# Kernel tuning notes

Measured on AMD Instinct MI355X. Metric: run time of the kernel, lower is better.

Reference implementation:

```python
import jax, jax.numpy as jnp
import numpy as np

DIM = 256   # state dimension
T = 8192    # number of time steps
B = 32      # batch of initial conditions
DT = 0.01   # time-grid spacing


def make_A(dim):
    # Faithful to MagnusLadder.__init__: diag=-0.1, superdiag=+0.5, subdiag=-0.5
    A = np.zeros((dim, dim), dtype=np.float32)
    np.fill_diagonal(A, -0.1)
    idx = np.arange(dim - 1)
    A[idx, idx + 1] = 0.5
    A[idx + 1, idx] = -0.5
    return jnp.asarray(A)


def setup_inputs() -> dict:
    key = jax.random.key(0)
    x0 = jax.random.normal(key, (DIM, B), dtype=jnp.float32)
    t = jnp.arange(T, dtype=jnp.float32) * DT  # uniform time grid, dt = DT
    A = make_A(DIM)
    return {"t": t, "x0": x0, "A": A}


def reference(t, x0, A):
    dt = t[1] - t[0]
    expAdt = jax.scipy.linalg.expm(A * dt)  # [dim, dim]

    def step(x, _):
        x = expAdt @ x  # [dim, B]
        return x, x

    _, traj = jax.lax.scan(step, x0, None, length=T - 1)  # [T-1, dim, B]
    return jnp.concatenate([x0[None], traj], axis=0)       # [T, dim, B]
```

## Files before the change

kernel.cpp:

```cpp
#include <hip/hip_runtime.h>
#include <hip/hip_bf16.h>


#define DIMN 256
#define BB   32
#define TSTEPS 8192
#define KT   32
#define DTF  0.01f

typedef __attribute__((ext_vector_type(8))) short bf16x8;
typedef __attribute__((ext_vector_type(4))) float f32x4;

static __device__ __forceinline__ short f2bf(float f) {
    union { __hip_bfloat16 h; short s; } u;
    u.h = __float2bfloat16(f);
    return u.s;
}

__global__ __launch_bounds__(256) void k1_prep(const float* __restrict__ x0,
                                               unsigned short* __restrict__ vfold,
                                               float* __restrict__ yr,
                                               float* __restrict__ yi) {
    const float PI257 = (float)(3.14159265358979323846 / 257.0);
    const float S257  = sqrtf(2.0f / 257.0f);
    const int g = blockIdx.x;
    const int t = threadIdx.x;

    __shared__ float x0s[256 * 32];
    __shared__ float ve[256], vo[256];
    __shared__ float psr[8][32], psi[8][32];

    if (g < 256) {
        const int j = g, J = j >> 1, p = j & 1, m = t;
        const int n = ((j + 1) * (m + 1)) % 514;
        const float v = S257 * sinf((float)n * PI257);
        float sgn;
        if (p == 0) sgn = (J & 1) ? -1.f : 1.f;
        else        sgn = (J & 1) ?  1.f : -1.f;
        vfold[p * 32768 + J * 256 + m] = (unsigned short)f2bf(sgn * v);
    } else {
        const int m = g - 256;
        for (int idx = t; idx < 256 * 32; idx += 256) x0s[idx] = x0[idx];
        const int n = ((m + 1) * (t + 1)) % 514;
        const float v = S257 * sinf((float)n * PI257);
        const int j = t;
        float veJ = 0.f, voJ = 0.f;
        if ((j & 1) == 0) veJ = ((j & 3) == 0) ? v : -v;
        else              voJ = ((j & 3) == 3) ? v : -v;
        ve[j] = veJ; vo[j] = voJ;
        __syncthreads();
        const int b = t & 31, jg = t >> 5;
        float sr = 0.f, si = 0.f;
#pragma unroll
        for (int jj2 = 0; jj2 < 32; ++jj2) {
            const int jj = jg * 32 + jj2;
            sr += ve[jj] * x0s[jj * 32 + b];
            si += vo[jj] * x0s[jj * 32 + b];
        }
        psr[jg][b] = sr; psi[jg][b] = si;
        __syncthreads();
        if (t < 32) {
            float asr = 0.f, asi = 0.f;
#pragma unroll
            for (int q = 0; q < 8; ++q) { asr += psr[q][t]; asi += psi[q][t]; }
            yr[m * 32 + t] = asr;
            yi[m * 32 + t] = asi;
        }
    }
}

__global__ __launch_bounds__(512, 2) void k2_main(const unsigned short* __restrict__ vfold,
                                                  const float* __restrict__ yr,
                                                  const float* __restrict__ yi,
                                                  float* __restrict__ out) {
    __shared__ unsigned short ubuf[2][2][2][8192];
    const float PI257   = (float)(3.14159265358979323846 / 257.0);
    const float INV2PI  = (float)(1.0 / (2.0 * 3.14159265358979323846));
    const int tid  = threadIdx.x;
    const int lane = tid & 63;
    const int wave = tid >> 6;
    const int k0   = blockIdx.x * KT;

    const int bA   = tid & 15;
    const int mblk = tid >> 4;
    const int m0   = mblk << 3;

    float threv[8], yrv0[8], yiv0[8], yrv1[8], yiv1[8];
#pragma unroll
    for (int i = 0; i < 8; ++i) {
        const int m = m0 + i;
        const float lam = cosf((float)(m + 1) * PI257);
        threv[i] = DTF * lam * INV2PI;
        yrv0[i] = yr[m * 32 + bA];       yiv0[i] = yi[m * 32 + bA];
        yrv1[i] = yr[m * 32 + bA + 16];  yiv1[i] = yi[m * 32 + bA + 16];
    }
    const int C0    = (mblk & 24) + ((mblk ^ (bA & 7)) & 7);
    const int wOff0 = bA * 256 + C0 * 8;
    const int wOff1 = wOff0 + 16 * 256;

    const int p  = wave & 1;
    const int wp = wave >> 1;
    const int rA = lane & 15;
    const int gA = lane >> 4;
    const int rl7 = rA & 7;

    bf16x8 bfrv[2][8];
#pragma unroll
    for (int ntile = 0; ntile < 2; ++ntile) {
        const unsigned short* vrow =
            vfold + p * 32768 + (wp * 32 + ntile * 16 + rA) * 256 + gA * 8;
#pragma unroll
        for (int ks = 0; ks < 8; ++ks)
            bfrv[ntile][ks] = *reinterpret_cast<const bf16x8*>(vrow + ks * 32);
    }

    float dec = expf(-0.001f * (float)k0);
    const float decr = expf(-0.001f);

    for (int r = 0; r < KT / 2; ++r) {
        const int d = r & 1;
#pragma unroll
        for (int kw = 0; kw < 2; ++kw) {
            const float kf = (float)(k0 + 2 * r + kw);
            bf16x8 vur0, vui0, vur1, vui1;
#pragma unroll
            for (int i = 0; i < 8; ++i) {
                const float ang = kf * threv[i];
                const float fr  = ang - floorf(ang);
                const float c   = __builtin_amdgcn_cosf(fr);
                const float s   = __builtin_amdgcn_sinf(fr);
                vur0[i] = f2bf(c * yrv0[i] - s * yiv0[i]);
                vui0[i] = f2bf(c * yiv0[i] + s * yrv0[i]);
                vur1[i] = f2bf(c * yrv1[i] - s * yiv1[i]);
                vui1[i] = f2bf(c * yiv1[i] + s * yrv1[i]);
            }
            *reinterpret_cast<bf16x8*>(&ubuf[d][kw][0][wOff0]) = vur0;
            *reinterpret_cast<bf16x8*>(&ubuf[d][kw][1][wOff0]) = vui0;
            *reinterpret_cast<bf16x8*>(&ubuf[d][kw][0][wOff1]) = vur1;
            *reinterpret_cast<bf16x8*>(&ubuf[d][kw][1][wOff1]) = vui1;
        }
        __syncthreads();

#pragma unroll
        for (int kw = 0; kw < 2; ++kw) {
            const unsigned short* up = &ubuf[d][kw][p][0];
            float* outk = out + (size_t)(k0 + 2 * r + kw) * 8192;
            f32x4 acc[2][2];
#pragma unroll
            for (int mt = 0; mt < 2; ++mt)
#pragma unroll
                for (int ntile = 0; ntile < 2; ++ntile)
                    acc[mt][ntile] = (f32x4){0.f, 0.f, 0.f, 0.f};
#pragma unroll
            for (int ks = 0; ks < 8; ++ks) {
                const int mo = ks * 4 + gA;
                const int csw = (mo & 24) + ((mo ^ rl7) & 7);
#pragma unroll
                for (int mt = 0; mt < 2; ++mt) {
                    const bf16x8 afr = *reinterpret_cast<const bf16x8*>(
                        up + (mt * 16 + rA) * 256 + csw * 8);
#pragma unroll
                    for (int ntile = 0; ntile < 2; ++ntile)
                        acc[mt][ntile] = __builtin_amdgcn_mfma_f32_16x16x32_bf16(
                            afr, bfrv[ntile][ks], acc[mt][ntile], 0, 0, 0);
                }
            }
#pragma unroll
            for (int ntile = 0; ntile < 2; ++ntile) {
                const int j = 2 * (wp * 32 + ntile * 16 + rA) + p;
#pragma unroll
                for (int mt = 0; mt < 2; ++mt) {
                    f32x4 v4;
#pragma unroll
                    for (int q = 0; q < 4; ++q) v4[q] = acc[mt][ntile][q] * dec;
                    *reinterpret_cast<f32x4*>(&outk[j * 32 + mt * 16 + gA * 4]) = v4;
                }
            }
            dec *= decr;
        }
    }
}

extern "C" void kernel_launch(void* const* d_in, const int* in_sizes, int n_in,
                              void* d_out, int out_size, void* d_ws, size_t ws_size,
                              hipStream_t stream) {
    const float* x0 = (const float*)d_in[1];
    float* out = (float*)d_out;

    unsigned short* vfold = (unsigned short*)d_ws;
    float* yr = (float*)((char*)d_ws + 131072);
    float* yi = (float*)((char*)d_ws + 131072 + 32768);

    k1_prep<<<512, 256, 0, stream>>>(x0, vfold, yr, yi);
    k2_main<<<256, 512, 0, stream>>>(vfold, yr, yi, out);
}
```

Measured before the change: 274.4 us.

## Halve LDS and registers per block to double occupancy, reload y from global

Halves the time steps per block (KT 32→16) and launches twice as many blocks, processing one time step per barrier instead of two. The LDS buffer shrinks to half, and the per-thread y coefficients are no longer held in registers. They are re-read each step from a transposed global layout with vectorized loads, and launch bounds are raised to 4 blocks per CU. It also replaces __syncthreads with a manual lgkmcnt wait plus s_barrier. The aim is more resident waves to hide the output store bandwidth, at the cost of repeated global/L2 loads of y and twice the barrier count per step.

New measurement: 315.6 us. 15.0% more time.

```diff
diff --git a/kernel.cpp b/kernel.cpp
--- a/kernel.cpp
+++ b/kernel.cpp
@@ -5,7 +5,7 @@
 #define DIMN 256
 #define BB   32
 #define TSTEPS 8192
-#define KT   32
+#define KT   16
 #define DTF  0.01f
 
 typedef __attribute__((ext_vector_type(8))) short bf16x8;
@@ -19,8 +19,7 @@
 
 __global__ __launch_bounds__(256) void k1_prep(const float* __restrict__ x0,
                                                unsigned short* __restrict__ vfold,
-                                               float* __restrict__ yr,
-                                               float* __restrict__ yi) {
+                                               float* __restrict__ yT) {
     const float PI257 = (float)(3.14159265358979323846 / 257.0);
     const float S257  = sqrtf(2.0f / 257.0f);
     const int g = blockIdx.x;
@@ -63,17 +62,16 @@
             float asr = 0.f, asi = 0.f;
 #pragma unroll
             for (int q = 0; q < 8; ++q) { asr += psr[q][t]; asi += psi[q][t]; }
-            yr[m * 32 + t] = asr;
-            yi[m * 32 + t] = asi;
+            yT[t * 256 + m]        = asr;
+            yT[8192 + t * 256 + m] = asi;
         }
     }
 }
 
-__global__ __launch_bounds__(512, 2) void k2_main(const unsigned short* __restrict__ vfold,
-                                                  const float* __restrict__ yr,
-                                                  const float* __restrict__ yi,
+__global__ __launch_bounds__(512, 4) void k2_main(const unsigned short* __restrict__ vfold,
+                                                  const float* __restrict__ yT,
                                                   float* __restrict__ out) {
-    __shared__ unsigned short ubuf[2][2][2][8192];
+    __shared__ unsigned short ubuf[2][2][8192];
     const float PI257   = (float)(3.14159265358979323846 / 257.0);
     const float INV2PI  = (float)(1.0 / (2.0 * 3.14159265358979323846));
     const int tid  = threadIdx.x;
@@ -85,23 +83,19 @@
     const int mblk = tid >> 4;
     const int m0   = mblk << 3;
 
-    float threv[8], yrv0[8], yiv0[8], yrv1[8], yiv1[8];
-#pragma unroll
-    for (int i = 0; i < 8; ++i) {
-        const int m = m0 + i;
-        const float lam = cosf((float)(m + 1) * PI257);
-        threv[i] = DTF * lam * INV2PI;
-        yrv0[i] = yr[m * 32 + bA];       yiv0[i] = yi[m * 32 + bA];
-        yrv1[i] = yr[m * 32 + bA + 16];  yiv1[i] = yi[m * 32 + bA + 16];
-    }
+    float threv[8];
+#pragma unroll
+    for (int i = 0; i < 8; ++i)
+        threv[i] = DTF * cosf((float)(m0 + i + 1) * PI257) * INV2PI;
+
     const int C0    = (mblk & 24) + ((mblk ^ (bA & 7)) & 7);
     const int wOff0 = bA * 256 + C0 * 8;
     const int wOff1 = wOff0 + 16 * 256;
 
-    const int p  = wave & 1;
-    const int wp = wave >> 1;
-    const int rA = lane & 15;
-    const int gA = lane >> 4;
+    const int p   = wave & 1;
+    const int wp  = wave >> 1;
+    const int rA  = lane & 15;
+    const int gA  = lane >> 4;
     const int rl7 = rA & 7;
 
     bf16x8 bfrv[2][8];
@@ -117,34 +111,47 @@
     float dec = expf(-0.001f * (float)k0);
     const float decr = expf(-0.001f);
 
-    for (int r = 0; r < KT / 2; ++r) {
+    for (int r = 0; r < KT; ++r) {
         const int d = r & 1;
-#pragma unroll
-        for (int kw = 0; kw < 2; ++kw) {
-            const float kf = (float)(k0 + 2 * r + kw);
-            bf16x8 vur0, vui0, vur1, vui1;
+        {
+            const float kf = (float)(k0 + r);
+            const float* yb = yT;
+            asm volatile("" : "+v"(yb));
+            float c[8], s[8];
 #pragma unroll
             for (int i = 0; i < 8; ++i) {
                 const float ang = kf * threv[i];
                 const float fr  = ang - floorf(ang);
-                const float c   = __builtin_amdgcn_cosf(fr);
-                const float s   = __builtin_amdgcn_sinf(fr);
-                vur0[i] = f2bf(c * yrv0[i] - s * yiv0[i]);
-                vui0[i] = f2bf(c * yiv0[i] + s * yrv0[i]);
-                vur1[i] = f2bf(c * yrv1[i] - s * yiv1[i]);
-                vui1[i] = f2bf(c * yiv1[i] + s * yrv1[i]);
-            }
-            *reinterpret_cast<bf16x8*>(&ubuf[d][kw][0][wOff0]) = vur0;
-            *reinterpret_cast<bf16x8*>(&ubuf[d][kw][1][wOff0]) = vui0;
-            *reinterpret_cast<bf16x8*>(&ubuf[d][kw][0][wOff1]) = vur1;
-            *reinterpret_cast<bf16x8*>(&ubuf[d][kw][1][wOff1]) = vui1;
-        }
-        __syncthreads();
-
-#pragma unroll
-        for (int kw = 0; kw < 2; ++kw) {
-            const unsigned short* up = &ubuf[d][kw][p][0];
-            float* outk = out + (size_t)(k0 + 2 * r + kw) * 8192;
+                c[i] = __builtin_amdgcn_cosf(fr);
+                s[i] = __builtin_amdgcn_sinf(fr);
+            }
+#pragma unroll
+            for (int col = 0; col < 2; ++col) {
+                const int boff = (bA + col * 16) * 256 + m0;
+                const f32x4 r0 = *reinterpret_cast<const f32x4*>(yb + boff);
+                const f32x4 r1 = *reinterpret_cast<const f32x4*>(yb + boff + 4);
+                const f32x4 i0 = *reinterpret_cast<const f32x4*>(yb + 8192 + boff);
+                const f32x4 i1 = *reinterpret_cast<const f32x4*>(yb + 8192 + boff + 4);
+                bf16x8 vur, vui;
+#pragma unroll
+                for (int i = 0; i < 4; ++i) {
+                    vur[i]     = f2bf(c[i] * r0[i] - s[i] * i0[i]);
+                    vui[i]     = f2bf(c[i] * i0[i] + s[i] * r0[i]);
+                    vur[4 + i] = f2bf(c[4 + i] * r1[i] - s[4 + i] * i1[i]);
+                    vui[4 + i] = f2bf(c[4 + i] * i1[i] + s[4 + i] * r1[i]);
+                }
+                const int wo = col ? wOff1 : wOff0;
+                *reinterpret_cast<bf16x8*>(&ubuf[d][0][wo]) = vur;
+                *reinterpret_cast<bf16x8*>(&ubuf[d][1][wo]) = vui;
+            }
+        }
+
+        asm volatile("s_waitcnt lgkmcnt(0)" ::: "memory");
+        __builtin_amdgcn_s_barrier();
+
+        {
+            const unsigned short* up = &ubuf[d][p][0];
+            float* outk = out + (size_t)(k0 + r) * 8192;
             f32x4 acc[2][2];
 #pragma unroll
             for (int mt = 0; mt < 2; ++mt)
@@ -153,7 +160,7 @@
                     acc[mt][ntile] = (f32x4){0.f, 0.f, 0.f, 0.f};
 #pragma unroll
             for (int ks = 0; ks < 8; ++ks) {
-                const int mo = ks * 4 + gA;
+                const int mo  = ks * 4 + gA;
                 const int csw = (mo & 24) + ((mo ^ rl7) & 7);
 #pragma unroll
                 for (int mt = 0; mt < 2; ++mt) {
@@ -188,9 +195,8 @@
     float* out = (float*)d_out;
 
     unsigned short* vfold = (unsigned short*)d_ws;
-    float* yr = (float*)((char*)d_ws + 131072);
-    float* yi = (float*)((char*)d_ws + 131072 + 32768);
-
-    k1_prep<<<512, 256, 0, stream>>>(x0, vfold, yr, yi);
-    k2_main<<<256, 512, 0, stream>>>(vfold, yr, yi, out);
-}
+    float* yT = (float*)((char*)d_ws + 131072);
+
+    k1_prep<<<512, 256, 0, stream>>>(x0, vfold, yT);
+    k2_main<<<512, 512, 0, stream>>>(vfold, yT, out);
+}
```
